# Optimization experiments

Measured on AMD Instinct MI355X. Metric: run time of the kernel, lower is better.

Reference implementation:

```python
import jax, jax.numpy as jnp
import numpy as np

T, NINP, NSTATE, NCH, NLAYER, NCLASS = 8192, 128, 1024, 4, 3, 10
GH = NSTATE // NCH  # per-channel GRU hidden size
EPS = 1e-5


def setup_inputs() -> dict:
    key = jax.random.key(0)
    ks = jax.random.split(key, 32)
    rn = lambda k, shape, scale: (jax.random.normal(k, shape, jnp.float32) * scale)
    he = lambda k, shape: rn(k, shape, (2.0 / shape[-1]) ** 0.5)
    # log_s per layer/channel: scale = 10**i for channel i
    log_s = jnp.log(10.0 ** jnp.arange(NCH, dtype=jnp.float32))[None, :, None]
    inp = {
        "inputs": rn(ks[0], (T, NINP), 1.0),
        "h0": jnp.zeros((GH,), jnp.float32),
        "yinit_guess": jnp.zeros((T, GH), jnp.float32),
        # encoder MLP (ninp -> nstate -> nstate), he_uniform-like init, zero bias
        "enc_w1": he(ks[1], (NSTATE, NINP)),
        "enc_b1": jnp.zeros((NSTATE,), jnp.float32),
        "enc_w2": he(ks[2], (NSTATE, NSTATE)),
        "enc_b2": jnp.zeros((NSTATE,), jnp.float32),
        # per-layer, per-channel GRU params
        "gru_wih": rn(ks[3], (NLAYER, NCH, 3 * GH, NSTATE), NSTATE ** -0.5),  # lecun_normal
        "gru_whh": rn(ks[4], (NLAYER, NCH, 3 * GH, GH), GH ** -0.5),  # stand-in for orthogonal
        "gru_b": jnp.zeros((NLAYER, NCH, 3 * GH), jnp.float32),
        "gru_bn": jnp.zeros((NLAYER, NCH, GH), jnp.float32),
        "gru_log_s": jnp.broadcast_to(log_s, (NLAYER, NCH, 1)).astype(jnp.float32),
        # per-layer residual MLPs (nstate -> nstate -> nstate)
        "mlp_w1": he(ks[5], (NLAYER, NSTATE, NSTATE)),
        "mlp_b1": jnp.zeros((NLAYER, NSTATE), jnp.float32),
        "mlp_w2": he(ks[6], (NLAYER, NSTATE, NSTATE)),
        "mlp_b2": jnp.zeros((NLAYER, NSTATE), jnp.float32),
        # classifier MLP (nstate -> nstate -> nclass)
        "cls_w1": he(ks[7], (NSTATE, NSTATE)),
        "cls_b1": jnp.zeros((NSTATE,), jnp.float32),
        "cls_w2": he(ks[8], (NCLASS, NSTATE)),
        "cls_b2": jnp.zeros((NCLASS,), jnp.float32),
    }
    return inp


def layernorm(x):  # weightless/bias-less LayerNorm over last dim
    m = jnp.mean(x, axis=-1, keepdims=True)
    v = jnp.var(x, axis=-1, keepdims=True)
    return (x - m) / jnp.sqrt(v + EPS)


def mlp(x, w1, b1, w2, b2):  # eqx.nn.MLP depth=1, relu
    h = jax.nn.relu(x @ w1.T + b1)
    return h @ w2.T + b2


def scale_gru_channel(wih, whh, b, bn, log_s, x, h0):
    # ScaleGRU recurrence: per step hnew = GRU(x_t/s, h); h' = (hnew - h)/s + h.
    # This is the exact fixed point that seq1d (DEER) converges to; yinit_guess
    # only affects convergence speed, not the result.
    s = jnp.exp(jnp.clip(log_s, -10.0, 10.0))[0]
    ig = (x / s) @ wih.T + b  # [T, 3*GH], input gates precomputed (parallel GEMM)

    def step(h, ig_t):
        hg = whh @ h  # [3*GH]
        r = jax.nn.sigmoid(ig_t[:GH] + hg[:GH])
        z = jax.nn.sigmoid(ig_t[GH:2 * GH] + hg[GH:2 * GH])
        n = jnp.tanh(ig_t[2 * GH:] + r * (hg[2 * GH:] + bn))
        hnew = n + z * (h - n)  # equinox GRUCell output
        hout = (hnew - h) / s + h  # ScaleGRU rescaling
        return hout, hout

    _, ys = jax.lax.scan(step, h0, ig)
    return ys  # [T, GH]


def reference(inputs, h0, yinit_guess, enc_w1, enc_b1, enc_w2, enc_b2,
              gru_wih, gru_whh, gru_b, gru_bn, gru_log_s,
              mlp_w1, mlp_b1, mlp_w2, mlp_b2,
              cls_w1, cls_b1, cls_w2, cls_b2):
    del yinit_guess  # initial guess for the DEER solver; exact solution is independent of it
    x = mlp(inputs, enc_w1, enc_b1, enc_w2, enc_b2)  # encoder: [T, NSTATE]
    run_channels = jax.vmap(scale_gru_channel, in_axes=(0, 0, 0, 0, 0, None, None))
    for i in range(NLAYER):
        xi = layernorm(x)  # norms[i]
        ch = run_channels(gru_wih[i], gru_whh[i], gru_b[i], gru_bn[i],
                          gru_log_s[i], xi, h0)  # [NCH, T, GH]
        y = jnp.transpose(ch, (1, 0, 2)).reshape(T, NSTATE)  # concat channels on last dim
        y = layernorm(y + xi)  # norms[i+1]
        x = mlp(y, mlp_w1[i], mlp_b1[i], mlp_w2[i], mlp_b2[i]) + y
    return mlp(x, cls_w1, cls_b1, cls_w2, cls_b2)  # [T, NCLASS]
```

## Files before the change

### kernel.cpp

```cpp
#include <hip/hip_runtime.h>

#define T_SEQ  8192
#define NST    1024
#define GHH    256
#define LD_IG  3072
#define C_CH   1024
#define NCHUNK 8
#define NDIAG  10

typedef _Float16 half8 __attribute__((ext_vector_type(8)));
typedef float f32x4 __attribute__((ext_vector_type(4)));

#define MFMA16(a, b, c) __builtin_amdgcn_mfma_f32_16x16x32_f16(a, b, c, 0, 0, 0)

__device__ __forceinline__ float sigmoid_f(float x) {
  return 1.0f / (1.0f + __expf(-x));
}
__device__ __forceinline__ float tanh_f(float x) {
  float ax = fabsf(x);
  float e = __expf(-2.0f * ax);
  float t = (1.0f - e) / (1.0f + e);
  return copysignf(t, x);
}

__global__ __launch_bounds__(256) void prep_whh(const float* __restrict__ whh,
                                                half8* __restrict__ wB)
{
  const int idx = blockIdx.x * 256 + threadIdx.x;
  const int lc  = idx / 24576;
  const int rem = idx - lc * 24576;
  const int g_id = rem >> 6, l = rem & 63;
  const int nb = g_id >> 3, kc = g_id & 7;
  const int g = nb >> 4, ub = nb & 15;
  const int n = l & 15, kg = l >> 4;
  const int row = g * 256 + ub * 16 + n;
  const int col = kc * 32 + kg * 8;
  const float* src = whh + (size_t)lc * 196608 + (size_t)row * 256 + col;
  float4 x0 = *reinterpret_cast<const float4*>(src);
  float4 x1 = *reinterpret_cast<const float4*>(src + 4);
  half8 o;
  o[0] = (_Float16)x0.x; o[1] = (_Float16)x0.y;
  o[2] = (_Float16)x0.z; o[3] = (_Float16)x0.w;
  o[4] = (_Float16)x1.x; o[5] = (_Float16)x1.y;
  o[6] = (_Float16)x1.z; o[7] = (_Float16)x1.w;
  wB[idx] = o;
}

__global__ __launch_bounds__(256) void cvt_to_h(const float* __restrict__ src,
                                                _Float16* __restrict__ dst, int n8)
{
  const int i = blockIdx.x * 256 + threadIdx.x;
  if (i >= n8) return;
  float4 a = reinterpret_cast<const float4*>(src)[2 * i];
  float4 b = reinterpret_cast<const float4*>(src)[2 * i + 1];
  half8 o;
  o[0] = (_Float16)a.x; o[1] = (_Float16)a.y; o[2] = (_Float16)a.z; o[3] = (_Float16)a.w;
  o[4] = (_Float16)b.x; o[5] = (_Float16)b.y; o[6] = (_Float16)b.z; o[7] = (_Float16)b.w;
  reinterpret_cast<half8*>(dst)[i] = o;
}

template<int EPI, bool RELU>
__global__ __launch_bounds__(256) void gemm_h(
    const float* __restrict__ A, const _Float16* __restrict__ Wh,
    const float* __restrict__ bias, const float* __restrict__ R,
    float* __restrict__ C, int M, int N, int K,
    const float* __restrict__ log_s)
{
  __shared__ _Float16 As[64][40];
  __shared__ _Float16 Ws[64][40];
  const int t = threadIdx.x;
  const int bm = blockIdx.x * 64, bn = blockIdx.y * 64;
  const int wave = t >> 6, l = t & 63;
  const int wm = (wave & 1) * 32, wn = (wave >> 1) * 32;
  const int sr = t >> 2, sc = (t & 3) * 8;
  const int fr = l & 15, fk = (l >> 4) * 8;

  f32x4 acc00 = {0.f, 0.f, 0.f, 0.f}, acc01 = acc00, acc10 = acc00, acc11 = acc00;

  const float* Ap     = A  + (size_t)(bm + sr) * K + sc;
  const _Float16* Wp  = Wh + (size_t)(bn + sr) * K + sc;

  for (int k0 = 0; k0 < K; k0 += 32) {
    float4 a0 = *reinterpret_cast<const float4*>(Ap + k0);
    float4 a1 = *reinterpret_cast<const float4*>(Ap + k0 + 4);
    half8 av;
    av[0] = (_Float16)a0.x; av[1] = (_Float16)a0.y;
    av[2] = (_Float16)a0.z; av[3] = (_Float16)a0.w;
    av[4] = (_Float16)a1.x; av[5] = (_Float16)a1.y;
    av[6] = (_Float16)a1.z; av[7] = (_Float16)a1.w;
    *reinterpret_cast<half8*>(&As[sr][sc]) = av;
    *reinterpret_cast<half8*>(&Ws[sr][sc]) =
        *reinterpret_cast<const half8*>(Wp + k0);
    __syncthreads();
    half8 af0 = *reinterpret_cast<const half8*>(&As[wm + fr][fk]);
    half8 af1 = *reinterpret_cast<const half8*>(&As[wm + 16 + fr][fk]);
    half8 bf0 = *reinterpret_cast<const half8*>(&Ws[wn + fr][fk]);
    half8 bf1 = *reinterpret_cast<const half8*>(&Ws[wn + 16 + fr][fk]);
    acc00 = MFMA16(af0, bf0, acc00);
    acc01 = MFMA16(af0, bf1, acc01);
    acc10 = MFMA16(af1, bf0, acc10);
    acc11 = MFMA16(af1, bf1, acc11);
    __syncthreads();
  }

#define EPI_STORE(ac, mi, ni) { \
    const int n_ = bn + wn + (ni) * 16 + fr; \
    const float bv = bias[n_]; \
    float sc_ = 1.f; \
    if (EPI == 1) { \
      float lsv = log_s[n_ / 768]; \
      lsv = fminf(fmaxf(lsv, -10.f), 10.f); \
      sc_ = __expf(-lsv); \
    } \
    _Pragma("unroll") \
    for (int q = 0; q < 4; ++q) { \
      const int m_ = bm + wm + (mi) * 16 + (l >> 4) * 4 + q; \
      float v = ac[q]; \
      if (EPI == 1) v *= sc_; \
      v += bv; \
      if (EPI == 2) v += R[(size_t)m_ * N + n_]; \
      if (RELU) v = fmaxf(v, 0.f); \
      C[(size_t)m_ * N + n_] = v; \
    } }
  EPI_STORE(acc00, 0, 0) EPI_STORE(acc01, 0, 1)
  EPI_STORE(acc10, 1, 0) EPI_STORE(acc11, 1, 1)
#undef EPI_STORE
}

template<bool ADD>
__global__ __launch_bounds__(256) void ln_kernel(const float* __restrict__ X,
                                                 const float* __restrict__ Yad,
                                                 float* __restrict__ O)
{
  const int row = blockIdx.x, t = threadIdx.x;
  float4 v = reinterpret_cast<const float4*>(X + (size_t)row * NST)[t];
  if (ADD) {
    float4 w = reinterpret_cast<const float4*>(Yad + (size_t)row * NST)[t];
    v.x += w.x; v.y += w.y; v.z += w.z; v.w += w.w;
  }
  float s  = v.x + v.y + v.z + v.w;
  float ss = v.x * v.x + v.y * v.y + v.z * v.z + v.w * v.w;
#pragma unroll
  for (int m = 1; m < 64; m <<= 1) {
    s  += __shfl_xor(s, m, 64);
    ss += __shfl_xor(ss, m, 64);
  }
  __shared__ float ps[4], pss[4];
  const int wv = t >> 6;
  if ((t & 63) == 0) { ps[wv] = s; pss[wv] = ss; }
  __syncthreads();
  s  = ps[0] + ps[1] + ps[2] + ps[3];
  ss = pss[0] + pss[1] + pss[2] + pss[3];
  const float mean = s * (1.f / 1024.f);
  const float var  = ss * (1.f / 1024.f) - mean * mean;
  const float rstd = rsqrtf(var + 1e-5f);
  v.x = (v.x - mean) * rstd; v.y = (v.y - mean) * rstd;
  v.z = (v.z - mean) * rstd; v.w = (v.w - mean) * rstd;
  reinterpret_cast<float4*>(O + (size_t)row * NST)[t] = v;
}

__global__ __launch_bounds__(256) void ln2_kernel(const float* __restrict__ Y,
                                                  const float* __restrict__ X,
                                                  float* __restrict__ O)
{
  const int row = blockIdx.x, t = threadIdx.x;
  const int wv = t >> 6;
  __shared__ float ps[4], pss[4], ps2[4], pss2[4];

  float4 xv = reinterpret_cast<const float4*>(X + (size_t)row * NST)[t];
  float s  = xv.x + xv.y + xv.z + xv.w;
  float ss = xv.x * xv.x + xv.y * xv.y + xv.z * xv.z + xv.w * xv.w;
#pragma unroll
  for (int m = 1; m < 64; m <<= 1) {
    s += __shfl_xor(s, m, 64); ss += __shfl_xor(ss, m, 64);
  }
  if ((t & 63) == 0) { ps[wv] = s; pss[wv] = ss; }
  __syncthreads();
  s = ps[0] + ps[1] + ps[2] + ps[3];
  ss = pss[0] + pss[1] + pss[2] + pss[3];
  float mean = s * (1.f / 1024.f);
  float var  = ss * (1.f / 1024.f) - mean * mean;
  float rstd = rsqrtf(var + 1e-5f);

  float4 yv = reinterpret_cast<const float4*>(Y + (size_t)row * NST)[t];
  float4 v;
  v.x = yv.x + (xv.x - mean) * rstd;
  v.y = yv.y + (xv.y - mean) * rstd;
  v.z = yv.z + (xv.z - mean) * rstd;
  v.w = yv.w + (xv.w - mean) * rstd;

  s  = v.x + v.y + v.z + v.w;
  ss = v.x * v.x + v.y * v.y + v.z * v.z + v.w * v.w;
#pragma unroll
  for (int m = 1; m < 64; m <<= 1) {
    s += __shfl_xor(s, m, 64); ss += __shfl_xor(ss, m, 64);
  }
  if ((t & 63) == 0) { ps2[wv] = s; pss2[wv] = ss; }
  __syncthreads();
  s = ps2[0] + ps2[1] + ps2[2] + ps2[3];
  ss = pss2[0] + pss2[1] + pss2[2] + pss2[3];
  mean = s * (1.f / 1024.f);
  var  = ss * (1.f / 1024.f) - mean * mean;
  rstd = rsqrtf(var + 1e-5f);
  v.x = (v.x - mean) * rstd; v.y = (v.y - mean) * rstd;
  v.z = (v.z - mean) * rstd; v.w = (v.w - mean) * rstd;
  reinterpret_cast<float4*>(O + (size_t)row * NST)[t] = v;
}

#define SCAN_BAR() asm volatile("s_waitcnt lgkmcnt(0)\n\ts_barrier" ::: "memory")

#define DECLB(i) half8 B##i##_0, B##i##_1, B##i##_2, B##i##_3, \
                       B##i##_4, B##i##_5, B##i##_6, B##i##_7;
#define LOADB(i) \
  B##i##_0 = wp[((i)*8+0)*64]; B##i##_1 = wp[((i)*8+1)*64]; \
  B##i##_2 = wp[((i)*8+2)*64]; B##i##_3 = wp[((i)*8+3)*64]; \
  B##i##_4 = wp[((i)*8+4)*64]; B##i##_5 = wp[((i)*8+5)*64]; \
  B##i##_6 = wp[((i)*8+6)*64]; B##i##_7 = wp[((i)*8+7)*64];

#define KCSTEP(kc) { \
  half8 a = hp[(kc) * 4]; \
  a0 = MFMA16(a, B0_##kc, a0); a1 = MFMA16(a, B1_##kc, a1); \
  a2 = MFMA16(a, B2_##kc, a2); a3 = MFMA16(a, B3_##kc, a3); \
  a4 = MFMA16(a, B4_##kc, a4); a5 = MFMA16(a, B5_##kc, a5); }

__global__ __attribute__((amdgpu_flat_work_group_size(512, 512)))
void scan_diag(
    const half8* __restrict__ wB,
    const float* __restrict__ gbn,
    const float* __restrict__ gls,
    const float* __restrict__ igb,
    const float* __restrict__ h0,
    float* __restrict__ hst,
    float* __restrict__ yb,
    int d)
{
  const int lidx = blockIdx.x >> 2;
  const int ch   = blockIdx.x & 3;
  const int c    = d - lidx;
  if (c < 0 || c >= NCHUNK) return;

  const int j = threadIdx.x;
  const int w = j >> 6, l = j & 63;
  const int lc = lidx * 4 + ch;
  const float* igc = igb + (size_t)lidx * (C_CH * LD_IG) + ch * 768;
  float* yc        = yb + (size_t)lidx * (C_CH * NST) + ch * GHH;

  const half8* wp = wB + (size_t)lc * 24576 + (size_t)(w * 48) * 64 + l;
  DECLB(0) DECLB(1) DECLB(2) DECLB(3) DECLB(4) DECLB(5)
  LOADB(0) LOADB(1) LOADB(2) LOADB(3) LOADB(4) LOADB(5)

  __shared__ __align__(16) _Float16 hsl[GHH];
  __shared__ float hg[768];

  const bool gate = (j < 256);
  float ls = gls[lc];
  ls = fminf(fmaxf(ls, -10.f), 10.f);
  const float inv_s = __expf(-ls);
  float bnj = 0.f, h = 0.f, ir = 0.f, iz = 0.f, in_ = 0.f;
  if (gate) {
    h   = (c == 0) ? h0[j] : hst[lc * GHH + j];
    bnj = gbn[lc * GHH + j];
    hsl[j] = (_Float16)h;
    ir = igc[j]; iz = igc[256 + j]; in_ = igc[512 + j];
  }
  SCAN_BAR();

  const half8* hp = reinterpret_cast<const half8*>(hsl) + (l >> 4);

  for (int t = 0; t < C_CH; ++t) {
    float nr = 0.f, nz = 0.f, nn = 0.f;
    if (gate && t + 1 < C_CH) {
      const float* p = igc + (size_t)(t + 1) * LD_IG;
      nr = p[j]; nz = p[256 + j]; nn = p[512 + j];
    }
    f32x4 a0 = {0.f, 0.f, 0.f, 0.f}, a1 = a0, a2 = a0, a3 = a0, a4 = a0, a5 = a0;
    KCSTEP(0) KCSTEP(1) KCSTEP(2) KCSTEP(3)
    KCSTEP(4) KCSTEP(5) KCSTEP(6) KCSTEP(7)
    if (l < 16) {
      hg[(w * 6 + 0) * 16 + l] = a0[0];
      hg[(w * 6 + 1) * 16 + l] = a1[0];
      hg[(w * 6 + 2) * 16 + l] = a2[0];
      hg[(w * 6 + 3) * 16 + l] = a3[0];
      hg[(w * 6 + 4) * 16 + l] = a4[0];
      hg[(w * 6 + 5) * 16 + l] = a5[0];
    }
    SCAN_BAR();
    if (gate) {
      const float hr = hg[j], hz = hg[256 + j], hn = hg[512 + j];
      const float rg = sigmoid_f(ir + hr);
      const float zg = sigmoid_f(iz + hz);
      const float ng = tanh_f(in_ + rg * (hn + bnj));
      const float hnew = ng + zg * (h - ng);
      h = (hnew - h) * inv_s + h;
      yc[(size_t)t * NST + j] = h;
      hsl[j] = (_Float16)h;
    }
    SCAN_BAR();
    ir = nr; iz = nz; in_ = nn;
  }
  if (gate) hst[lc * GHH + j] = h;
}

__global__ __launch_bounds__(256) void gemv_cls(const float* __restrict__ A,
                                                const float* __restrict__ W,
                                                const float* __restrict__ b,
                                                float* __restrict__ out)
{
  const int m = blockIdx.x, t = threadIdx.x;
  float4 a = reinterpret_cast<const float4*>(A + (size_t)m * NST)[t];
  float p[10];
#pragma unroll
  for (int n = 0; n < 10; ++n) {
    float4 w = reinterpret_cast<const float4*>(W + (size_t)n * NST)[t];
    p[n] = a.x * w.x + a.y * w.y + a.z * w.z + a.w * w.w;
  }
#pragma unroll
  for (int n = 0; n < 10; ++n)
#pragma unroll
    for (int msk = 1; msk < 64; msk <<= 1) p[n] += __shfl_xor(p[n], msk, 64);
  __shared__ float red[4][10];
  const int wv = t >> 6;
  if ((t & 63) == 0) {
#pragma unroll
    for (int n = 0; n < 10; ++n) red[wv][n] = p[n];
  }
  __syncthreads();
  if (t < 10) {
    float v = red[0][t] + red[1][t] + red[2][t] + red[3][t] + b[t];
    out[(size_t)m * 10 + t] = v;
  }
}

extern "C" void kernel_launch(void* const* d_in, const int* in_sizes, int n_in,
                              void* d_out, int out_size, void* d_ws, size_t ws_size,
                              hipStream_t stream) {
  const float* inputs = (const float*)d_in[0];
  const float* h0     = (const float*)d_in[1];
  const float* enc_w1 = (const float*)d_in[3];
  const float* enc_b1 = (const float*)d_in[4];
  const float* enc_w2 = (const float*)d_in[5];
  const float* enc_b2 = (const float*)d_in[6];
  const float* gwih   = (const float*)d_in[7];
  const float* gwhh   = (const float*)d_in[8];
  const float* gb     = (const float*)d_in[9];
  const float* gbn    = (const float*)d_in[10];
  const float* gls    = (const float*)d_in[11];
  const float* mw1    = (const float*)d_in[12];
  const float* mb1    = (const float*)d_in[13];
  const float* mw2    = (const float*)d_in[14];
  const float* mb2    = (const float*)d_in[15];
  const float* cw1    = (const float*)d_in[16];
  const float* cb1    = (const float*)d_in[17];
  const float* cw2    = (const float*)d_in[18];
  const float* cb2    = (const float*)d_in[19];
  float* out = (float*)d_out;

  char* ws = (char*)d_ws;
  float* x0    = (float*)(ws);
  float* xr1   = (float*)(ws + 33554432ull);
  float* xr2   = (float*)(ws + 41943040ull);
  float* igbuf = (float*)(ws + 50331648ull);
  half8* gw16  = (half8*)(ws + 88080384ull);
  float* bufY  = (float*)(ws + 92798976ull);
  float* bufYn = (float*)(ws + 105381888ull);
  float* bufH  = (float*)(ws + 109576192ull);
  float* xitmp = (float*)(ws + 113770496ull);
  float* xf    = (float*)(ws + 117964800ull);
  float* clsH  = (float*)(ws + 122159104ull);
  float* hst   = (float*)(ws + 126353408ull);
  _Float16* wf = (_Float16*)(ws + 126365696ull);

  _Float16* wh_enc1 = wf;
  _Float16* wh_enc2 = wf + 131072;
  _Float16* wh_wih  = wf + 1179648;
  _Float16* wh_mw1  = wf + 10616832;
  _Float16* wh_mw2  = wf + 13762560;
  _Float16* wh_cw1  = wf + 16908288;

  const dim3 blk(256);
  const dim3 g_enc(8192 / 64, 1024 / 64);
  const dim3 g_ig(C_CH / 64, 3072 / 64);
  const dim3 g_mlp(C_CH / 64, 1024 / 64);

  auto xptr = [&](int lth, int c) -> float* {
    if (lth == 0) return x0 + (size_t)c * C_CH * NST;
    float* base = (lth == 1) ? xr1 : xr2;
    return base + (size_t)(c & 1) * C_CH * NST;
  };

  prep_whh<<<dim3(1152), blk, 0, stream>>>(gwhh, gw16);
  cvt_to_h<<<dim3(64),   blk, 0, stream>>>(enc_w1, wh_enc1, 16384);
  cvt_to_h<<<dim3(512),  blk, 0, stream>>>(enc_w2, wh_enc2, 131072);
  cvt_to_h<<<dim3(4608), blk, 0, stream>>>(gwih,   wh_wih,  1179648);
  cvt_to_h<<<dim3(1536), blk, 0, stream>>>(mw1,    wh_mw1,  393216);
  cvt_to_h<<<dim3(1536), blk, 0, stream>>>(mw2,    wh_mw2,  393216);
  cvt_to_h<<<dim3(512),  blk, 0, stream>>>(cw1,    wh_cw1,  131072);

  gemm_h<0, true ><<<g_enc, blk, 0, stream>>>(inputs, wh_enc1, enc_b1, nullptr,
                                              (float*)igbuf, 8192, 1024, 128, nullptr);
  gemm_h<0, false><<<g_enc, blk, 0, stream>>>((float*)igbuf, wh_enc2, enc_b2, nullptr,
                                              x0, 8192, 1024, 1024, nullptr);

  for (int d = 0; d < NDIAG; ++d) {
    for (int lth = 0; lth < 3; ++lth) {
      const int c = d - lth;
      if (c < 0 || c >= NCHUNK) continue;
      ln_kernel<false><<<dim3(C_CH), blk, 0, stream>>>(xptr(lth, c), nullptr, xitmp);
      gemm_h<1, false><<<g_ig, blk, 0, stream>>>(
          xitmp, wh_wih + (size_t)lth * 3145728, gb + (size_t)lth * 3072,
          nullptr, igbuf + (size_t)lth * C_CH * LD_IG, C_CH, 3072, 1024,
          gls + (size_t)lth * 4);
    }
    scan_diag<<<dim3(12), dim3(512), 0, stream>>>(gw16, gbn, gls, igbuf,
                                                  h0, hst, bufY, d);
    for (int lth = 0; lth < 3; ++lth) {
      const int c = d - lth;
      if (c < 0 || c >= NCHUNK) continue;
      ln2_kernel<<<dim3(C_CH), blk, 0, stream>>>(
          bufY + (size_t)lth * C_CH * NST, xptr(lth, c), bufYn);
      gemm_h<0, true ><<<g_mlp, blk, 0, stream>>>(
          bufYn, wh_mw1 + (size_t)lth * 1048576, mb1 + (size_t)lth * 1024,
          nullptr, bufH, C_CH, 1024, 1024, nullptr);
      float* xnext = (lth < 2) ? xptr(lth + 1, c) : xf;
      gemm_h<2, false><<<g_mlp, blk, 0, stream>>>(
          bufH, wh_mw2 + (size_t)lth * 1048576, mb2 + (size_t)lth * 1024,
          bufYn, xnext, C_CH, 1024, 1024, nullptr);
      if (lth == 2) {
        gemm_h<0, true><<<g_mlp, blk, 0, stream>>>(
            xf, wh_cw1, cb1, nullptr, clsH, C_CH, 1024, 1024, nullptr);
        gemv_cls<<<dim3(C_CH), blk, 0, stream>>>(clsH, cw2, cb2,
                                                 out + (size_t)c * C_CH * 10);
      }
    }
  }
}
```

Baseline: 13.28 ms.

## Halve scan chunk size and fuse gate math into MFMA lanes with double-buffered state

The sequence is split into 16 chunks of 512 instead of 8 chunks of 1024, so the layer-wavefront pipeline has more diagonals and shorter fill and drain. In the scan kernel, the weight slices are reassigned so that each wave's accumulators hold the r, z and n rows for the same hidden units. The gate nonlinearity can then run directly on the MFMA lanes, with no shared-memory staging. Double-buffering the fp16 hidden state removes one of the two barriers per timestep, at the cost of doing the gate work on only 16 lanes per wave, more kernel launches, and a reshuffled workspace layout.

```diff
diff --git a/kernel.cpp b/kernel.cpp
--- a/kernel.cpp
+++ b/kernel.cpp
@@ -4,9 +4,9 @@
 #define NST    1024
 #define GHH    256
 #define LD_IG  3072
-#define C_CH   1024
-#define NCHUNK 8
-#define NDIAG  10
+#define C_CH   512
+#define NCHUNK 16
+#define NDIAG  18
 
 typedef _Float16 half8 __attribute__((ext_vector_type(8)));
 typedef float f32x4 __attribute__((ext_vector_type(4)));
@@ -211,11 +211,11 @@
 
 #define DECLB(i) half8 B##i##_0, B##i##_1, B##i##_2, B##i##_3, \
                        B##i##_4, B##i##_5, B##i##_6, B##i##_7;
-#define LOADB(i) \
-  B##i##_0 = wp[((i)*8+0)*64]; B##i##_1 = wp[((i)*8+1)*64]; \
-  B##i##_2 = wp[((i)*8+2)*64]; B##i##_3 = wp[((i)*8+3)*64]; \
-  B##i##_4 = wp[((i)*8+4)*64]; B##i##_5 = wp[((i)*8+5)*64]; \
-  B##i##_6 = wp[((i)*8+6)*64]; B##i##_7 = wp[((i)*8+7)*64];
+#define LOADBn(i, nb) \
+  B##i##_0 = wpB[((nb)*8+0)*64]; B##i##_1 = wpB[((nb)*8+1)*64]; \
+  B##i##_2 = wpB[((nb)*8+2)*64]; B##i##_3 = wpB[((nb)*8+3)*64]; \
+  B##i##_4 = wpB[((nb)*8+4)*64]; B##i##_5 = wpB[((nb)*8+5)*64]; \
+  B##i##_6 = wpB[((nb)*8+6)*64]; B##i##_7 = wpB[((nb)*8+7)*64];
 
 #define KCSTEP(kc) { \
   half8 a = hp[(kc) * 4]; \
@@ -245,60 +245,69 @@
   const float* igc = igb + (size_t)lidx * (C_CH * LD_IG) + ch * 768;
   float* yc        = yb + (size_t)lidx * (C_CH * NST) + ch * GHH;
 
-  const half8* wp = wB + (size_t)lc * 24576 + (size_t)(w * 48) * 64 + l;
+  const half8* wpB = wB + (size_t)lc * 24576 + l;
   DECLB(0) DECLB(1) DECLB(2) DECLB(3) DECLB(4) DECLB(5)
-  LOADB(0) LOADB(1) LOADB(2) LOADB(3) LOADB(4) LOADB(5)
-
-  __shared__ __align__(16) _Float16 hsl[GHH];
-  __shared__ float hg[768];
-
-  const bool gate = (j < 256);
+  LOADBn(0, w)      LOADBn(1, w + 8)  LOADBn(2, w + 16)
+  LOADBn(3, w + 24) LOADBn(4, w + 32) LOADBn(5, w + 40)
+
+  __shared__ __align__(16) _Float16 hsl[2][GHH];
+
+  const bool glane = (l < 16);
+  const int u1 = 16 * w + l;
+  const int u2 = 128 + 16 * w + l;
+
   float ls = gls[lc];
   ls = fminf(fmaxf(ls, -10.f), 10.f);
   const float inv_s = __expf(-ls);
-  float bnj = 0.f, h = 0.f, ir = 0.f, iz = 0.f, in_ = 0.f;
-  if (gate) {
-    h   = (c == 0) ? h0[j] : hst[lc * GHH + j];
-    bnj = gbn[lc * GHH + j];
-    hsl[j] = (_Float16)h;
-    ir = igc[j]; iz = igc[256 + j]; in_ = igc[512 + j];
+  float bn1 = 0.f, bn2 = 0.f, h1 = 0.f, h2 = 0.f;
+  float i1r = 0.f, i1z = 0.f, i1n = 0.f, i2r = 0.f, i2z = 0.f, i2n = 0.f;
+  if (glane) {
+    h1 = (c == 0) ? h0[u1] : hst[lc * GHH + u1];
+    h2 = (c == 0) ? h0[u2] : hst[lc * GHH + u2];
+    bn1 = gbn[lc * GHH + u1];
+    bn2 = gbn[lc * GHH + u2];
+    hsl[0][u1] = (_Float16)h1;
+    hsl[0][u2] = (_Float16)h2;
+    i1r = igc[u1]; i1z = igc[256 + u1]; i1n = igc[512 + u1];
+    i2r = igc[u2]; i2z = igc[256 + u2]; i2n = igc[512 + u2];
   }
   SCAN_BAR();
 
-  const half8* hp = reinterpret_cast<const half8*>(hsl) + (l >> 4);
-
   for (int t = 0; t < C_CH; ++t) {
-    float nr = 0.f, nz = 0.f, nn = 0.f;
-    if (gate && t + 1 < C_CH) {
+    float n1r = 0.f, n1z = 0.f, n1n = 0.f, n2r = 0.f, n2z = 0.f, n2n = 0.f;
+    if (glane && t + 1 < C_CH) {
       const float* p = igc + (size_t)(t + 1) * LD_IG;
-      nr = p[j]; nz = p[256 + j]; nn = p[512 + j];
+      n1r = p[u1]; n1z = p[256 + u1]; n1n = p[512 + u1];
+      n2r = p[u2]; n2z = p[256 + u2]; n2n = p[512 + u2];
     }
+    const half8* hp = reinterpret_cast<const half8*>(hsl[t & 1]) + (l >> 4);
     f32x4 a0 = {0.f, 0.f, 0.f, 0.f}, a1 = a0, a2 = a0, a3 = a0, a4 = a0, a5 = a0;
     KCSTEP(0) KCSTEP(1) KCSTEP(2) KCSTEP(3)
     KCSTEP(4) KCSTEP(5) KCSTEP(6) KCSTEP(7)
-    if (l < 16) {
-      hg[(w * 6 + 0) * 16 + l] = a0[0];
-      hg[(w * 6 + 1) * 16 + l] = a1[0];
-      hg[(w * 6 + 2) * 16 + l] = a2[0];
-      hg[(w * 6 + 3) * 16 + l] = a3[0];
-      hg[(w * 6 + 4) * 16 + l] = a4[0];
-      hg[(w * 6 + 5) * 16 + l] = a5[0];
+    if (glane) {
+      const float rg1 = sigmoid_f(i1r + a0[0]);
+      const float zg1 = sigmoid_f(i1z + a2[0]);
+      const float ng1 = tanh_f(i1n + rg1 * (a4[0] + bn1));
+      const float hw1 = ng1 + zg1 * (h1 - ng1);
+      h1 = (hw1 - h1) * inv_s + h1;
+      const float rg2 = sigmoid_f(i2r + a1[0]);
+      const float zg2 = sigmoid_f(i2z + a3[0]);
+      const float ng2 = tanh_f(i2n + rg2 * (a5[0] + bn2));
+      const float hw2 = ng2 + zg2 * (h2 - ng2);
+      h2 = (hw2 - h2) * inv_s + h2;
+      yc[(size_t)t * NST + u1] = h1;
+      yc[(size_t)t * NST + u2] = h2;
+      hsl[(t + 1) & 1][u1] = (_Float16)h1;
+      hsl[(t + 1) & 1][u2] = (_Float16)h2;
     }
     SCAN_BAR();
-    if (gate) {
-      const float hr = hg[j], hz = hg[256 + j], hn = hg[512 + j];
-      const float rg = sigmoid_f(ir + hr);
-      const float zg = sigmoid_f(iz + hz);
-      const float ng = tanh_f(in_ + rg * (hn + bnj));
-      const float hnew = ng + zg * (h - ng);
-      h = (hnew - h) * inv_s + h;
-      yc[(size_t)t * NST + j] = h;
-      hsl[j] = (_Float16)h;
-    }
-    SCAN_BAR();
-    ir = nr; iz = nz; in_ = nn;
-  }
-  if (gate) hst[lc * GHH + j] = h;
+    i1r = n1r; i1z = n1z; i1n = n1n;
+    i2r = n2r; i2z = n2z; i2n = n2n;
+  }
+  if (glane) {
+    hst[lc * GHH + u1] = h1;
+    hst[lc * GHH + u2] = h2;
+  }
 }
 
 __global__ __launch_bounds__(256) void gemv_cls(const float* __restrict__ A,
@@ -358,17 +367,18 @@
   char* ws = (char*)d_ws;
   float* x0    = (float*)(ws);
   float* xr1   = (float*)(ws + 33554432ull);
-  float* xr2   = (float*)(ws + 41943040ull);
-  float* igbuf = (float*)(ws + 50331648ull);
-  half8* gw16  = (half8*)(ws + 88080384ull);
-  float* bufY  = (float*)(ws + 92798976ull);
-  float* bufYn = (float*)(ws + 105381888ull);
-  float* bufH  = (float*)(ws + 109576192ull);
-  float* xitmp = (float*)(ws + 113770496ull);
-  float* xf    = (float*)(ws + 117964800ull);
-  float* clsH  = (float*)(ws + 122159104ull);
-  float* hst   = (float*)(ws + 126353408ull);
-  _Float16* wf = (_Float16*)(ws + 126365696ull);
+  float* xr2   = (float*)(ws + 37748736ull);
+  float* igbuf = (float*)(ws + 41943040ull);
+  half8* gw16  = (half8*)(ws + 60817408ull);
+  float* bufY  = (float*)(ws + 65536000ull);
+  float* bufYn = (float*)(ws + 71827456ull);
+  float* bufH  = (float*)(ws + 73924608ull);
+  float* xitmp = (float*)(ws + 76021760ull);
+  float* xf    = (float*)(ws + 78118912ull);
+  float* clsH  = (float*)(ws + 80216064ull);
+  float* hst   = (float*)(ws + 82313216ull);
+  _Float16* wf = (_Float16*)(ws + 82325504ull);
+  float* encS  = (float*)(ws + 118239232ull);
 
   _Float16* wh_enc1 = wf;
   _Float16* wh_enc2 = wf + 131072;
@@ -397,8 +407,8 @@
   cvt_to_h<<<dim3(512),  blk, 0, stream>>>(cw1,    wh_cw1,  131072);
 
   gemm_h<0, true ><<<g_enc, blk, 0, stream>>>(inputs, wh_enc1, enc_b1, nullptr,
-                                              (float*)igbuf, 8192, 1024, 128, nullptr);
-  gemm_h<0, false><<<g_enc, blk, 0, stream>>>((float*)igbuf, wh_enc2, enc_b2, nullptr,
+                                              encS, 8192, 1024, 128, nullptr);
+  gemm_h<0, false><<<g_enc, blk, 0, stream>>>(encS, wh_enc2, enc_b2, nullptr,
                                               x0, 8192, 1024, 1024, nullptr);
 
   for (int d = 0; d < NDIAG; ++d) {
```

Result: slower. 16.21 ms (median of 3 runs) (+22.0%).

## Remap GRU scan weights so each wave owns its gates, removing a barrier

Applied to the files above, without the earlier changes.

Weight tiles are reassigned so each wave computes the r, z and n pre-activations for the same hidden units. Lanes can then apply the gate nonlinearity directly from MFMA accumulators instead of exchanging partial results through shared memory. The h vector is double-buffered in LDS, so one of the two barriers per timestep is removed. The cost is that only 32 lanes per wave do gate math, and correctness depends on the weight layout matching the new per-wave tile ownership.

```diff
diff --git a/kernel.cpp b/kernel.cpp
--- a/kernel.cpp
+++ b/kernel.cpp
@@ -211,11 +211,11 @@
 
 #define DECLB(i) half8 B##i##_0, B##i##_1, B##i##_2, B##i##_3, \
                        B##i##_4, B##i##_5, B##i##_6, B##i##_7;
-#define LOADB(i) \
-  B##i##_0 = wp[((i)*8+0)*64]; B##i##_1 = wp[((i)*8+1)*64]; \
-  B##i##_2 = wp[((i)*8+2)*64]; B##i##_3 = wp[((i)*8+3)*64]; \
-  B##i##_4 = wp[((i)*8+4)*64]; B##i##_5 = wp[((i)*8+5)*64]; \
-  B##i##_6 = wp[((i)*8+6)*64]; B##i##_7 = wp[((i)*8+7)*64];
+#define LOADBn(i, nb) \
+  B##i##_0 = wpB[((nb)*8+0)*64]; B##i##_1 = wpB[((nb)*8+1)*64]; \
+  B##i##_2 = wpB[((nb)*8+2)*64]; B##i##_3 = wpB[((nb)*8+3)*64]; \
+  B##i##_4 = wpB[((nb)*8+4)*64]; B##i##_5 = wpB[((nb)*8+5)*64]; \
+  B##i##_6 = wpB[((nb)*8+6)*64]; B##i##_7 = wpB[((nb)*8+7)*64];
 
 #define KCSTEP(kc) { \
   half8 a = hp[(kc) * 4]; \
@@ -245,60 +245,55 @@
   const float* igc = igb + (size_t)lidx * (C_CH * LD_IG) + ch * 768;
   float* yc        = yb + (size_t)lidx * (C_CH * NST) + ch * GHH;
 
-  const half8* wp = wB + (size_t)lc * 24576 + (size_t)(w * 48) * 64 + l;
+  const half8* wpB = wB + (size_t)lc * 24576 + l;
   DECLB(0) DECLB(1) DECLB(2) DECLB(3) DECLB(4) DECLB(5)
-  LOADB(0) LOADB(1) LOADB(2) LOADB(3) LOADB(4) LOADB(5)
-
-  __shared__ __align__(16) _Float16 hsl[GHH];
-  __shared__ float hg[768];
-
-  const bool gate = (j < 256);
+  LOADBn(0, w)      LOADBn(1, w + 8)  LOADBn(2, w + 16)
+  LOADBn(3, w + 24) LOADBn(4, w + 32) LOADBn(5, w + 40)
+
+  __shared__ __align__(16) _Float16 hsl[2][GHH];
+
+  const bool glane = (l < 32);
+  const bool hi    = (l & 16) != 0;
+  const int u = 16 * w + (l & 15) + (hi ? 128 : 0);
+
   float ls = gls[lc];
   ls = fminf(fmaxf(ls, -10.f), 10.f);
   const float inv_s = __expf(-ls);
-  float bnj = 0.f, h = 0.f, ir = 0.f, iz = 0.f, in_ = 0.f;
-  if (gate) {
-    h   = (c == 0) ? h0[j] : hst[lc * GHH + j];
-    bnj = gbn[lc * GHH + j];
-    hsl[j] = (_Float16)h;
-    ir = igc[j]; iz = igc[256 + j]; in_ = igc[512 + j];
+  float bnu = 0.f, h = 0.f, ir = 0.f, iz = 0.f, in_ = 0.f;
+  if (glane) {
+    h   = (c == 0) ? h0[u] : hst[lc * GHH + u];
+    bnu = gbn[lc * GHH + u];
+    hsl[0][u] = (_Float16)h;
+    ir = igc[u]; iz = igc[256 + u]; in_ = igc[512 + u];
   }
   SCAN_BAR();
-
-  const half8* hp = reinterpret_cast<const half8*>(hsl) + (l >> 4);
 
   for (int t = 0; t < C_CH; ++t) {
     float nr = 0.f, nz = 0.f, nn = 0.f;
-    if (gate && t + 1 < C_CH) {
+    if (glane && t + 1 < C_CH) {
       const float* p = igc + (size_t)(t + 1) * LD_IG;
-      nr = p[j]; nz = p[256 + j]; nn = p[512 + j];
+      nr = p[u]; nz = p[256 + u]; nn = p[512 + u];
     }
+    const half8* hp = reinterpret_cast<const half8*>(hsl[t & 1]) + (l >> 4);
     f32x4 a0 = {0.f, 0.f, 0.f, 0.f}, a1 = a0, a2 = a0, a3 = a0, a4 = a0, a5 = a0;
     KCSTEP(0) KCSTEP(1) KCSTEP(2) KCSTEP(3)
     KCSTEP(4) KCSTEP(5) KCSTEP(6) KCSTEP(7)
-    if (l < 16) {
-      hg[(w * 6 + 0) * 16 + l] = a0[0];
-      hg[(w * 6 + 1) * 16 + l] = a1[0];
-      hg[(w * 6 + 2) * 16 + l] = a2[0];
-      hg[(w * 6 + 3) * 16 + l] = a3[0];
-      hg[(w * 6 + 4) * 16 + l] = a4[0];
-      hg[(w * 6 + 5) * 16 + l] = a5[0];
-    }
-    SCAN_BAR();
-    if (gate) {
-      const float hr = hg[j], hz = hg[256 + j], hn = hg[512 + j];
-      const float rg = sigmoid_f(ir + hr);
-      const float zg = sigmoid_f(iz + hz);
-      const float ng = tanh_f(in_ + rg * (hn + bnj));
-      const float hnew = ng + zg * (h - ng);
-      h = (hnew - h) * inv_s + h;
-      yc[(size_t)t * NST + j] = h;
-      hsl[j] = (_Float16)h;
+    if (glane) {
+      const float pr = hi ? a1[0] : a0[0];
+      const float pz = hi ? a3[0] : a2[0];
+      const float pn = hi ? a5[0] : a4[0];
+      const float rg = sigmoid_f(ir + pr);
+      const float zg = sigmoid_f(iz + pz);
+      const float ng = tanh_f(in_ + rg * (pn + bnu));
+      const float hw = ng + zg * (h - ng);
+      h = (hw - h) * inv_s + h;
+      yc[(size_t)t * NST + u] = h;
+      hsl[(t + 1) & 1][u] = (_Float16)h;
     }
     SCAN_BAR();
     ir = nr; iz = nz; in_ = nn;
   }
-  if (gate) hst[lc * GHH + j] = h;
+  if (glane) hst[lc * GHH + u] = h;
 }
 
 __global__ __launch_bounds__(256) void gemv_cls(const float* __restrict__ A,
```

Result: faster. 12.04 ms (-9.3%).
